# Kernel optimization log

Hardware: AMD Instinct MI355X
Metric: run time of the kernel (lower is better)

## Reference

```python
import jax, jax.numpy as jnp
import numpy as np

BUCKETS = 64
DIM = 512  # self.dim, used only for attention scaling


def setup_inputs() -> dict:
    key = jax.random.key(0)
    k1, k2, k3, k4 = jax.random.split(key, 4)
    b, h, t, dh = 4, 8, 8192, 64
    q = jax.random.normal(k1, (b, h, t, dh), dtype=jnp.float32)
    k = jax.random.normal(k2, (b, h, t, dh), dtype=jnp.float32)
    v = jax.random.normal(k3, (b, h, t, dh), dtype=jnp.float32)
    W = jax.random.normal(k4, (1, h, 2 * dh, BUCKETS), dtype=jnp.float32)  # SimpleSortNet.linear
    return {"q": q, "k": k, "v": v, "W": W}


def reference(q, k, v, W):
    b, h, t, dh = q.shape
    bh = b * h
    bsz = t // BUCKETS  # bucket size = 128

    # merge batch and heads, then bucket: [bh, buckets, bsz, dh]
    b_q = q.reshape(bh, BUCKETS, bsz, dh)
    b_k = k.reshape(bh, BUCKETS, bsz, dh)
    b_v = v.reshape(bh, BUCKETS, bsz, dh)

    # --- SimpleSortNet (non_permutative=True -> softmax, no gumbel) ---
    # summarize each bucket by sum over tokens, concat q/k summaries
    x = jnp.concatenate([b_q.sum(axis=2), b_k.sum(axis=2)], axis=-1)  # [bh, buckets, 2*dh]
    Wb = jnp.broadcast_to(W, (b, h, 2 * dh, BUCKETS)).reshape(bh, 2 * dh, BUCKETS)
    R = jax.nn.relu(jnp.einsum('bud,bdv->buv', x, Wb))  # [bh, buckets, buckets]
    R = jax.nn.softmax(R, axis=-1)

    # zero_all_but_top: keep only top-1 entry along last dim (dim=2)
    top_idx = jnp.argmax(R, axis=-1)  # [bh, buckets]
    top_mask = jnp.arange(BUCKETS) == top_idx[..., None]
    R = jnp.where(top_mask, R, jnp.zeros((), dtype=R.dtype))

    # reorder key/value buckets by (sparsified) R
    b_k_r = jnp.einsum('buv,bvtd->butd', R, b_k)
    b_v_r = jnp.einsum('buv,bvtd->butd', R, b_v)

    # buckets == kv_buckets: attend over [reordered bucket ; own bucket]
    bk = jnp.concatenate([b_k_r, b_k], axis=2)  # [bh, buckets, 2*bsz, dh]
    bv = jnp.concatenate([b_v_r, b_v], axis=2)

    # bucketed attention; note: original scales by self.dim ** -0.5 (full dim)
    dots = jnp.einsum('buie,buje->buij', b_q, bk) * (DIM ** -0.5)
    attn = jax.nn.softmax(dots, axis=-1)
    out = jnp.einsum('buij,buje->buie', attn, bv)  # [bh, buckets, bsz, dh]

    return out.reshape(b, h, t, dh)
```

## Files before the change

### kernel.cpp

```cpp
#include <hip/hip_runtime.h>


#define T_TOK 8192
#define CQ (0.04419417382415922f * 1.4426950408889634f)
#define FIXED_M 12.0f

#define KB_OFF 0
#define VT_OFF 65536
#undef VT_OFF
#define VT_OFF 32768
#define XB_OFF 65536
#define QP_OFF 66048
#define KP_OFF 67072

typedef __attribute__((ext_vector_type(16))) float f32x16;
typedef __attribute__((ext_vector_type(8))) short bf16x8;

__device__ __forceinline__ unsigned cvtpk(float lo, float hi) {
  unsigned r;
  asm("v_cvt_pk_bf16_f32 %0, %1, %2" : "=v"(r) : "v"(lo), "v"(hi));
  return r;
}
__device__ __forceinline__ float exp2v(float x) {
  float r;
  asm("v_exp_f32 %0, %1\n\ts_nop 0" : "=v"(r) : "v"(x));
  return r;
}

__global__ __launch_bounds__(256, 2) void k3_attn(
    const float* __restrict__ q, const float* __restrict__ k,
    const float* __restrict__ v, const float* __restrict__ W,
    float* __restrict__ out) {
  __shared__ unsigned char smem[71168];

  int L = blockIdx.x;
  int G = ((L & 7) << 8) | (L >> 3);
  int bhi = G >> 6, u = G & 63;
  int tid = threadIdx.x;
  int l = tid & 63;
  int w = tid >> 6;
  int lhi = l >> 5;
  int ln = l & 31;
  int hh = bhi & 7;

  const float* kb = k + (size_t)bhi * (T_TOK * 64);
  const float* vb = v + (size_t)bhi * (T_TOK * 64);

  const float* qrow = q + ((size_t)bhi * T_TOK + (size_t)u * 128 + w * 32 + ln) * 64;
  bf16x8 qf[4];
  float qs[32];
  #pragma unroll
  for (int sl = 0; sl < 4; ++sl) {
    float4 a4 = *reinterpret_cast<const float4*>(qrow + sl * 16 + lhi * 8);
    float4 b4 = *reinterpret_cast<const float4*>(qrow + sl * 16 + lhi * 8 + 4);
    qs[sl * 8 + 0] = a4.x; qs[sl * 8 + 1] = a4.y;
    qs[sl * 8 + 2] = a4.z; qs[sl * 8 + 3] = a4.w;
    qs[sl * 8 + 4] = b4.x; qs[sl * 8 + 5] = b4.y;
    qs[sl * 8 + 6] = b4.z; qs[sl * 8 + 7] = b4.w;
    union { unsigned uu[4]; bf16x8 f; } qu;
    qu.uu[0] = cvtpk(a4.x * CQ, a4.y * CQ);
    qu.uu[1] = cvtpk(a4.z * CQ, a4.w * CQ);
    qu.uu[2] = cvtpk(b4.x * CQ, b4.y * CQ);
    qu.uu[3] = cvtpk(b4.z * CQ, b4.w * CQ);
    qf[sl] = qu.f;
  }
  #pragma unroll
  for (int off = 1; off < 32; off <<= 1) {
    #pragma unroll
    for (int j = 0; j < 32; ++j) qs[j] += __shfl_xor(qs[j], off, 64);
  }
  if (ln == 0) {
    float* qp = (float*)(smem + QP_OFF) + w * 64 + lhi * 8;
    #pragma unroll
    for (int sl = 0; sl < 4; ++sl) {
      #pragma unroll
      for (int j = 0; j < 8; ++j) qp[sl * 16 + j] = qs[sl * 8 + j];
    }
  }

  int c4 = tid & 15;
  float4 ksum = make_float4(0.f, 0.f, 0.f, 0.f);
  #pragma unroll
  for (int it = 0; it < 8; ++it) {
    int row = (tid >> 4) + it * 16;
    float4 val = *reinterpret_cast<const float4*>(
        kb + (size_t)(u * 128 + row) * 64 + c4 * 4);
    ksum.x += val.x; ksum.y += val.y; ksum.z += val.z; ksum.w += val.w;
    int lr = 128 + row;
    int addr = KB_OFF + lr * 128 + ((c4 * 8) ^ ((lr & 7) << 4));
    *reinterpret_cast<uint2*>(smem + addr) =
        make_uint2(cvtpk(val.x, val.y), cvtpk(val.z, val.w));
  }
  *reinterpret_cast<float4*>(smem + KP_OFF + tid * 16) = ksum;

  int tp = tid >> 2;
  {
    const float* s0 = vb + ((size_t)(u * 128 + 2 * tp)) * 64 + (tid & 3) * 4;
    #pragma unroll
    for (int i = 0; i < 4; ++i) {
      int dq = (tid & 3) + 4 * i;
      float4 va = *reinterpret_cast<const float4*>(s0 + i * 16);
      float4 vc = *reinterpret_cast<const float4*>(s0 + i * 16 + 64);
      int t2 = 256 + 4 * tp;
      const float* fa = (const float*)&va;
      const float* fc = (const float*)&vc;
      #pragma unroll
      for (int jj = 0; jj < 4; ++jj) {
        int d = dq * 4 + jj;
        int addr = VT_OFF + d * 512 + (t2 ^ ((d & 31) << 4));
        *reinterpret_cast<unsigned*>(smem + addr) = cvtpk(fa[jj], fc[jj]);
      }
    }
  }

  __syncthreads();

  if (tid < 64) {
    const float* qp = (const float*)(smem + QP_OFF);
    float xq = qp[tid] + qp[64 + tid] + qp[128 + tid] + qp[192 + tid];
    const float* kp = (const float*)(smem + KP_OFF);
    float xk = 0.f;
    #pragma unroll
    for (int g = 0; g < 16; ++g) xk += kp[(g * 16 + (tid >> 2)) * 4 + (tid & 3)];
    float* xbw = (float*)(smem + XB_OFF);
    xbw[tid] = xq;
    xbw[64 + tid] = xk;
  }
  __syncthreads();

  const float* xb = (const float*)(smem + XB_OFF);
  const float* wcol = W + (size_t)hh * 8192 + l;
  float a = 0.f;
  #pragma unroll 8
  for (int kk = 0; kk < 128; ++kk) a = fmaf(xb[kk], wcol[(size_t)kk * 64], a);
  a = fmaxf(a, 0.f);
  float bvv = a; int bi = l;
  #pragma unroll
  for (int off = 1; off < 64; off <<= 1) {
    float ov = __shfl_xor(bvv, off, 64);
    int oi = __shfl_xor(bi, off, 64);
    if (ov > bvv || (ov == bvv && oi < bi)) { bvv = ov; bi = oi; }
  }
  float e = __expf(a - bvv);
  #pragma unroll
  for (int off = 1; off < 64; off <<= 1) e += __shfl_xor(e, off, 64);
  int vu = bi;
  float ru = 1.f / e;

  #pragma unroll
  for (int it = 0; it < 8; ++it) {
    int row = (tid >> 4) + it * 16;
    float4 val = *reinterpret_cast<const float4*>(
        kb + (size_t)(vu * 128 + row) * 64 + c4 * 4);
    int addr = KB_OFF + row * 128 + ((c4 * 8) ^ ((row & 7) << 4));
    *reinterpret_cast<uint2*>(smem + addr) =
        make_uint2(cvtpk(val.x, val.y), cvtpk(val.z, val.w));
  }

  {
    const float* s0 = vb + ((size_t)(vu * 128 + 2 * tp)) * 64 + (tid & 3) * 4;
    #pragma unroll
    for (int i = 0; i < 4; ++i) {
      int dq = (tid & 3) + 4 * i;
      float4 va = *reinterpret_cast<const float4*>(s0 + i * 16);
      float4 vc = *reinterpret_cast<const float4*>(s0 + i * 16 + 64);
      int t2 = 4 * tp;
      const float* fa = (const float*)&va;
      const float* fc = (const float*)&vc;
      #pragma unroll
      for (int jj = 0; jj < 4; ++jj) {
        int d = dq * 4 + jj;
        int addr = VT_OFF + d * 512 + (t2 ^ ((d & 31) << 4));
        *reinterpret_cast<unsigned*>(smem + addr) = cvtpk(fa[jj] * ru, fc[jj] * ru);
      }
    }
  }

  __syncthreads();

  f32x16 o0, o1;
  #pragma unroll
  for (int r = 0; r < 16; ++r) { o0[r] = 0.f; o1[r] = 0.f; }
  float lsum = 0.f;

  #pragma unroll
  for (int t8 = 0; t8 < 8; ++t8) {
    int tokr = t8 * 32 + ln;

    f32x16 acc;
    #pragma unroll
    for (int r = 0; r < 16; ++r) acc[r] = 0.f;
    #pragma unroll
    for (int sl = 0; sl < 4; ++sl) {
      int addr = KB_OFF + tokr * 128 + ((sl * 32 + lhi * 16) ^ ((tokr & 7) << 4));
      bf16x8 af = *reinterpret_cast<const bf16x8*>(smem + addr);
      acc = __builtin_amdgcn_mfma_f32_32x32x16_bf16(af, qf[sl], acc, 0, 0, 0);
    }

    #pragma unroll
    for (int r = 0; r < 16; ++r) {
      float lg = (t8 < 4) ? acc[r] * ru : acc[r];
      float p = exp2v(lg - FIXED_M);
      acc[r] = p;
      lsum += p;
    }

    #pragma unroll
    for (int ks = 0; ks < 2; ++ks) {
      int r0 = 8 * ks;
      unsigned aA, bA, aB, bB;
      asm("v_cvt_pk_bf16_f32 %0, %1, %2" : "=v"(aA) : "v"(acc[r0 + 0]), "v"(acc[r0 + 1]));
      asm("v_cvt_pk_bf16_f32 %0, %1, %2" : "=v"(bA) : "v"(acc[r0 + 2]), "v"(acc[r0 + 3]));
      asm("v_cvt_pk_bf16_f32 %0, %1, %2" : "=v"(aB) : "v"(acc[r0 + 4]), "v"(acc[r0 + 5]));
      asm("v_cvt_pk_bf16_f32 %0, %1, %2" : "=v"(bB) : "v"(acc[r0 + 6]), "v"(acc[r0 + 7]));
      asm("s_nop 1\n\tv_permlane32_swap_b32 %0, %1\n\ts_nop 1" : "+v"(aA), "+v"(aB));
      asm("s_nop 1\n\tv_permlane32_swap_b32 %0, %1\n\ts_nop 1" : "+v"(bA), "+v"(bB));
      union { unsigned uu[4]; bf16x8 f; } pf;
      pf.uu[0] = aA; pf.uu[1] = bA; pf.uu[2] = aB; pf.uu[3] = bB;

      int t2 = 2 * (t8 * 32 + ks * 16 + lhi * 8);
      {
        int d = ln;
        int addr = VT_OFF + d * 512 + (t2 ^ ((d & 31) << 4));
        bf16x8 vf = *reinterpret_cast<const bf16x8*>(smem + addr);
        o0 = __builtin_amdgcn_mfma_f32_32x32x16_bf16(pf.f, vf, o0, 0, 0, 0);
      }
      {
        int d = 32 + ln;
        int addr = VT_OFF + d * 512 + (t2 ^ ((d & 31) << 4));
        bf16x8 vf = *reinterpret_cast<const bf16x8*>(smem + addr);
        o1 = __builtin_amdgcn_mfma_f32_32x32x16_bf16(pf.f, vf, o1, 0, 0, 0);
      }
    }
  }

  lsum += __shfl_xor(lsum, 32, 64);
  float inv = 1.f / lsum;
  float* ob = out + ((size_t)bhi * T_TOK + (size_t)u * 128 + w * 32) * 64;
  #pragma unroll
  for (int r = 0; r < 16; ++r) {
    int row = (r & 3) + 8 * (r >> 2) + 4 * lhi;
    float invr = __shfl(inv, row, 64);
    ob[(size_t)row * 64 + ln] = o0[r] * invr;
    ob[(size_t)row * 64 + 32 + ln] = o1[r] * invr;
  }
}

extern "C" void kernel_launch(void* const* d_in, const int* in_sizes, int n_in,
                              void* d_out, int out_size, void* d_ws, size_t ws_size,
                              hipStream_t stream) {
  const float* q = (const float*)d_in[0];
  const float* k = (const float*)d_in[1];
  const float* v = (const float*)d_in[2];
  const float* W = (const float*)d_in[3];
  float* out = (float*)d_out;

  hipLaunchKernelGGL(k3_attn, dim3(2048), dim3(256), 0, stream, q, k, v, W, out);
}
```

Baseline: 79.29 us.

## Overlap selected-bucket K/V loads with own-bucket attention tiles

Loads the selected (reordered) bucket's K and V into registers first, then computes attention over the own bucket already resident in LDS while those loads complete. After that it converts the selected bucket into LDS, synchronizes, and processes the remaining tiles. The aim is to hide global-memory latency for the second gather behind MFMA work and to remove one barrier stall. The cost is 64 extra live VGPRs across the first half of the attention, which risks spills or reduced occupancy under the two-blocks-per-CU launch bound.

```diff
diff --git a/kernel.cpp b/kernel.cpp
--- a/kernel.cpp
+++ b/kernel.cpp
@@ -6,8 +6,6 @@
 #define FIXED_M 12.0f
 
 #define KB_OFF 0
-#define VT_OFF 65536
-#undef VT_OFF
 #define VT_OFF 32768
 #define XB_OFF 65536
 #define QP_OFF 66048
@@ -26,6 +24,56 @@
   asm("v_exp_f32 %0, %1\n\ts_nop 0" : "=v"(r) : "v"(x));
   return r;
 }
+
+#define ATTN_TILE(T8, VUHALF)                                                  \
+  {                                                                            \
+    int tokr = (T8) * 32 + ln;                                                 \
+    f32x16 acc;                                                                \
+    _Pragma("unroll") for (int r = 0; r < 16; ++r) acc[r] = 0.f;               \
+    _Pragma("unroll") for (int sl = 0; sl < 4; ++sl) {                         \
+      int addr =                                                               \
+          KB_OFF + tokr * 128 + ((sl * 32 + lhi * 16) ^ ((tokr & 7) << 4));    \
+      bf16x8 af = *reinterpret_cast<const bf16x8*>(smem + addr);               \
+      acc = __builtin_amdgcn_mfma_f32_32x32x16_bf16(af, qf[sl], acc, 0, 0, 0); \
+    }                                                                          \
+    _Pragma("unroll") for (int r = 0; r < 16; ++r) {                           \
+      float lg = (VUHALF) ? acc[r] * ru : acc[r];                              \
+      float p = exp2v(lg - FIXED_M);                                           \
+      acc[r] = p;                                                              \
+      lsum += p;                                                               \
+    }                                                                          \
+    _Pragma("unroll") for (int ks = 0; ks < 2; ++ks) {                         \
+      int r0 = 8 * ks;                                                         \
+      unsigned aA, bA, aB, bB;                                                 \
+      asm("v_cvt_pk_bf16_f32 %0, %1, %2"                                       \
+          : "=v"(aA) : "v"(acc[r0 + 0]), "v"(acc[r0 + 1]));                    \
+      asm("v_cvt_pk_bf16_f32 %0, %1, %2"                                       \
+          : "=v"(bA) : "v"(acc[r0 + 2]), "v"(acc[r0 + 3]));                    \
+      asm("v_cvt_pk_bf16_f32 %0, %1, %2"                                       \
+          : "=v"(aB) : "v"(acc[r0 + 4]), "v"(acc[r0 + 5]));                    \
+      asm("v_cvt_pk_bf16_f32 %0, %1, %2"                                       \
+          : "=v"(bB) : "v"(acc[r0 + 6]), "v"(acc[r0 + 7]));                    \
+      asm("s_nop 1\n\tv_permlane32_swap_b32 %0, %1\n\ts_nop 1"                 \
+          : "+v"(aA), "+v"(aB));                                               \
+      asm("s_nop 1\n\tv_permlane32_swap_b32 %0, %1\n\ts_nop 1"                 \
+          : "+v"(bA), "+v"(bB));                                               \
+      union { unsigned uu[4]; bf16x8 f; } pf;                                  \
+      pf.uu[0] = aA; pf.uu[1] = bA; pf.uu[2] = aB; pf.uu[3] = bB;              \
+      int t2 = 2 * ((T8) * 32 + ks * 16 + lhi * 8);                            \
+      {                                                                        \
+        int d = ln;                                                            \
+        int addr = VT_OFF + d * 512 + (t2 ^ ((d & 31) << 4));                  \
+        bf16x8 vf = *reinterpret_cast<const bf16x8*>(smem + addr);             \
+        o0 = __builtin_amdgcn_mfma_f32_32x32x16_bf16(pf.f, vf, o0, 0, 0, 0);   \
+      }                                                                        \
+      {                                                                        \
+        int d = 32 + ln;                                                       \
+        int addr = VT_OFF + d * 512 + (t2 ^ ((d & 31) << 4));                  \
+        bf16x8 vf = *reinterpret_cast<const bf16x8*>(smem + addr);             \
+        o1 = __builtin_amdgcn_mfma_f32_32x32x16_bf16(pf.f, vf, o1, 0, 0, 0);   \
+      }                                                                        \
+    }                                                                          \
+  }
 
 __global__ __launch_bounds__(256, 2) void k3_attn(
     const float* __restrict__ q, const float* __restrict__ k,
@@ -147,92 +195,55 @@
   int vu = bi;
   float ru = 1.f / e;
 
+  float4 kvu[8];
   #pragma unroll
   for (int it = 0; it < 8; ++it) {
     int row = (tid >> 4) + it * 16;
-    float4 val = *reinterpret_cast<const float4*>(
+    kvu[it] = *reinterpret_cast<const float4*>(
         kb + (size_t)(vu * 128 + row) * 64 + c4 * 4);
+  }
+  float4 vvu[8];
+  {
+    const float* s0 = vb + ((size_t)(vu * 128 + 2 * tp)) * 64 + (tid & 3) * 4;
+    #pragma unroll
+    for (int i = 0; i < 4; ++i) {
+      vvu[i] = *reinterpret_cast<const float4*>(s0 + i * 16);
+      vvu[4 + i] = *reinterpret_cast<const float4*>(s0 + i * 16 + 64);
+    }
+  }
+
+  f32x16 o0, o1;
+  #pragma unroll
+  for (int r = 0; r < 16; ++r) { o0[r] = 0.f; o1[r] = 0.f; }
+  float lsum = 0.f;
+
+  #pragma unroll
+  for (int t8 = 4; t8 < 8; ++t8) ATTN_TILE(t8, false)
+
+  #pragma unroll
+  for (int it = 0; it < 8; ++it) {
+    int row = (tid >> 4) + it * 16;
     int addr = KB_OFF + row * 128 + ((c4 * 8) ^ ((row & 7) << 4));
     *reinterpret_cast<uint2*>(smem + addr) =
-        make_uint2(cvtpk(val.x, val.y), cvtpk(val.z, val.w));
-  }
-
-  {
-    const float* s0 = vb + ((size_t)(vu * 128 + 2 * tp)) * 64 + (tid & 3) * 4;
-    #pragma unroll
-    for (int i = 0; i < 4; ++i) {
-      int dq = (tid & 3) + 4 * i;
-      float4 va = *reinterpret_cast<const float4*>(s0 + i * 16);
-      float4 vc = *reinterpret_cast<const float4*>(s0 + i * 16 + 64);
-      int t2 = 4 * tp;
-      const float* fa = (const float*)&va;
-      const float* fc = (const float*)&vc;
-      #pragma unroll
-      for (int jj = 0; jj < 4; ++jj) {
-        int d = dq * 4 + jj;
-        int addr = VT_OFF + d * 512 + (t2 ^ ((d & 31) << 4));
-        *reinterpret_cast<unsigned*>(smem + addr) = cvtpk(fa[jj] * ru, fc[jj] * ru);
-      }
-    }
-  }
-
+        make_uint2(cvtpk(kvu[it].x, kvu[it].y), cvtpk(kvu[it].z, kvu[it].w));
+  }
+  #pragma unroll
+  for (int i = 0; i < 4; ++i) {
+    int dq = (tid & 3) + 4 * i;
+    int t2 = 4 * tp;
+    const float* fa = (const float*)&vvu[i];
+    const float* fc = (const float*)&vvu[4 + i];
+    #pragma unroll
+    for (int jj = 0; jj < 4; ++jj) {
+      int d = dq * 4 + jj;
+      int addr = VT_OFF + d * 512 + (t2 ^ ((d & 31) << 4));
+      *reinterpret_cast<unsigned*>(smem + addr) = cvtpk(fa[jj] * ru, fc[jj] * ru);
+    }
+  }
   __syncthreads();
 
-  f32x16 o0, o1;
-  #pragma unroll
-  for (int r = 0; r < 16; ++r) { o0[r] = 0.f; o1[r] = 0.f; }
-  float lsum = 0.f;
-
-  #pragma unroll
-  for (int t8 = 0; t8 < 8; ++t8) {
-    int tokr = t8 * 32 + ln;
-
-    f32x16 acc;
-    #pragma unroll
-    for (int r = 0; r < 16; ++r) acc[r] = 0.f;
-    #pragma unroll
-    for (int sl = 0; sl < 4; ++sl) {
-      int addr = KB_OFF + tokr * 128 + ((sl * 32 + lhi * 16) ^ ((tokr & 7) << 4));
-      bf16x8 af = *reinterpret_cast<const bf16x8*>(smem + addr);
-      acc = __builtin_amdgcn_mfma_f32_32x32x16_bf16(af, qf[sl], acc, 0, 0, 0);
-    }
-
-    #pragma unroll
-    for (int r = 0; r < 16; ++r) {
-      float lg = (t8 < 4) ? acc[r] * ru : acc[r];
-      float p = exp2v(lg - FIXED_M);
-      acc[r] = p;
-      lsum += p;
-    }
-
-    #pragma unroll
-    for (int ks = 0; ks < 2; ++ks) {
-      int r0 = 8 * ks;
-      unsigned aA, bA, aB, bB;
-      asm("v_cvt_pk_bf16_f32 %0, %1, %2" : "=v"(aA) : "v"(acc[r0 + 0]), "v"(acc[r0 + 1]));
-      asm("v_cvt_pk_bf16_f32 %0, %1, %2" : "=v"(bA) : "v"(acc[r0 + 2]), "v"(acc[r0 + 3]));
-      asm("v_cvt_pk_bf16_f32 %0, %1, %2" : "=v"(aB) : "v"(acc[r0 + 4]), "v"(acc[r0 + 5]));
-      asm("v_cvt_pk_bf16_f32 %0, %1, %2" : "=v"(bB) : "v"(acc[r0 + 6]), "v"(acc[r0 + 7]));
-      asm("s_nop 1\n\tv_permlane32_swap_b32 %0, %1\n\ts_nop 1" : "+v"(aA), "+v"(aB));
-      asm("s_nop 1\n\tv_permlane32_swap_b32 %0, %1\n\ts_nop 1" : "+v"(bA), "+v"(bB));
-      union { unsigned uu[4]; bf16x8 f; } pf;
-      pf.uu[0] = aA; pf.uu[1] = bA; pf.uu[2] = aB; pf.uu[3] = bB;
-
-      int t2 = 2 * (t8 * 32 + ks * 16 + lhi * 8);
-      {
-        int d = ln;
-        int addr = VT_OFF + d * 512 + (t2 ^ ((d & 31) << 4));
-        bf16x8 vf = *reinterpret_cast<const bf16x8*>(smem + addr);
-        o0 = __builtin_amdgcn_mfma_f32_32x32x16_bf16(pf.f, vf, o0, 0, 0, 0);
-      }
-      {
-        int d = 32 + ln;
-        int addr = VT_OFF + d * 512 + (t2 ^ ((d & 31) << 4));
-        bf16x8 vf = *reinterpret_cast<const bf16x8*>(smem + addr);
-        o1 = __builtin_amdgcn_mfma_f32_32x32x16_bf16(pf.f, vf, o1, 0, 0, 0);
-      }
-    }
-  }
+  #pragma unroll
+  for (int t8 = 0; t8 < 4; ++t8) ATTN_TILE(t8, true)
 
   lsum += __shfl_xor(lsum, 32, 64);
   float inv = 1.f / lsum;
```

Result: faster. 77.55 us (-2.2%).
